# Kernel tuning notes

Hardware: AMD Instinct MI355X
Metric: run time of the kernel (lower is better)

Reference implementation:

```python
import jax, jax.numpy as jnp
import numpy as np

K = 16                      # instance ids 1..K (0 = background, ignored)
DELTA_V, DELTA_D, GAMMA = 0.5, 1.5, 0.001
W_CLUST, W_CENTER, W_BOUND, W_LOVASZ = 0.1, 0.1, 0.05, 0.01


def _pdist(x, y):
    # x: [..., n, d], y: [..., m, d] -> euclidean distances [..., n, m]
    x2 = (x * x).sum(-1)[..., :, None]
    y2 = (y * y).sum(-1)[..., None, :]
    d2 = x2 + y2 - 2.0 * jnp.einsum('...nd,...md->...nm', x, y)
    return jnp.sqrt(jnp.maximum(d2, 0.0))


def _losses(points, embeddings, labels):
    # F.normalize(embeddings, p=2, dim=2)
    emb = embeddings / jnp.maximum(
        jnp.linalg.norm(embeddings, axis=-1, keepdims=True), 1e-12)
    B, N, D = emb.shape
    ids = jnp.arange(1, K + 1)
    M = (labels[..., None] == ids).astype(emb.dtype)            # [B,N,K]
    cnt = M.sum(1)                                               # [B,K] (>=1 by construction)
    # raw per-instance feature centers (mean of normalized embeddings)
    fc = jnp.einsum('bnk,bnd->bkd', M, emb) / cnt[..., None]     # [B,K,D]
    cen = fc / jnp.maximum(jnp.linalg.norm(fc, axis=-1, keepdims=True), 1e-12)

    # ---- clustering: variance term ----
    d_nc = _pdist(emb, cen)                                      # [B,N,K]
    var_loss = ((jnp.maximum(d_nc - DELTA_V, 0.0) * M).sum(1) / cnt).sum() / (B + 1e-6)

    # ---- clustering: inter-center distance term ----
    cd = _pdist(cen, cen)                                        # [B,K,K]
    off = 1.0 - jnp.eye(K, dtype=emb.dtype)
    dist_loss = ((jnp.maximum(2.0 * DELTA_D - cd, 0.0) * off).sum((1, 2))
                 / (K * (K - 1))).sum() / (B + 1e-6)

    # ---- clustering: regularizer (Frobenius norm of centers) ----
    reg_loss = jnp.linalg.norm(cen.reshape(B, -1), axis=1).sum() * GAMMA / (B + 1e-6)

    # ---- center loss: spatial dist * feature dist to per-instance means ----
    gc = jnp.einsum('bnk,bnc->bkc', M, points) / cnt[..., None]  # geometric centers [B,K,3]
    sd = _pdist(points, gc)                                      # [B,N,K]
    fd = _pdist(emb, fc)                                         # [B,N,K] (fc NOT renormalized)
    center_loss = ((sd * fd * M).sum(1) / cnt).sum() / B

    # ---- boundary loss: full NxN cdist, zero same-instance entries ----
    dm = _pdist(emb, emb)                                        # [B,N,N]
    same = labels[:, :, None] == labels[:, None, :]
    bd = dm * (~same).astype(emb.dtype)
    boundary_loss = jnp.maximum(DELTA_D - bd, 0.0).mean(axis=(1, 2)).sum() / B

    enorm = jnp.maximum(jnp.linalg.norm(emb, axis=-1), 1e-8)     # [B,N]
    mnorm = jnp.maximum(jnp.linalg.norm(fc, axis=-1), 1e-8)      # [B,K]
    sim = jnp.einsum('bnd,bkd->bnk', emb, fc) / (enorm[..., None] * mnorm[:, None, :])
    order = jnp.argsort(-sim, axis=1)                            # descending sort per (b,k)
    ss = jnp.take_along_axis(sim, order, axis=1)                 # sorted similarities
    sm = jnp.take_along_axis(M, order, axis=1)                   # masks in sorted order
    inter = cnt[:, None, :] - jnp.cumsum(sm, axis=1)
    union = cnt[:, None, :] + jnp.cumsum(1.0 - sm, axis=1)
    jac = 1.0 - inter / union
    jd = jnp.concatenate([jac[:, :1], jac[:, 1:] - jac[:, :-1]], axis=1)
    lovasz_loss = (jnp.maximum(ss, 0.0) * jd).sum() / B

    total = (W_CLUST * (var_loss + dist_loss + reg_loss)
             + W_CENTER * center_loss + W_BOUND * boundary_loss
             + W_LOVASZ * lovasz_loss)
    return jnp.stack([total, var_loss, dist_loss, reg_loss,
                      center_loss, boundary_loss, lovasz_loss])


def setup_inputs() -> dict:
    key = jax.random.key(0)
    k1, k2, k3 = jax.random.split(key, 3)
    B, N, D = 4, 4096, 64
    points = jax.random.normal(k1, (B, N, 3), jnp.float32)
    embeddings = jax.random.normal(k2, (B, N, D), jnp.float32)
    labels = jax.random.randint(k3, (B, N), 0, K + 1)
    # guarantee every id 0..K appears in each cloud (matches torch unique() set)
    labels = labels.at[:, :K + 1].set(jnp.arange(K + 1))
    return {"points": points, "embeddings": embeddings, "instance_labels": labels}


def reference(points, embeddings, instance_labels):
    # returns stacked [total, var, dist, reg, center, boundary, lovasz]
    return _losses(points, embeddings, instance_labels)
```

## Files before the change

kernel.cpp:

```cpp
#include <hip/hip_runtime.h>

#define BB 4
#define NN 4096
#define DD 64
#define KK 16
#define NBUCK 2048
#define NCHB 144
#define NBND (NCHB * BB)
#define NLV1 256

#define OFF_EMB   0u
#define OFF_NRM2  1048576u
#define OFF_PFC   1064960u
#define OFF_PGC   1327104u
#define OFF_PCNT  1339392u
#define OFF_FC    1343488u
#define OFF_CEN   1347584u
#define OFF_GC    1351680u
#define OFF_FCN   1351872u
#define OFF_FCN2  1351936u
#define OFF_CEN2  1352000u
#define OFF_GC2   1352064u
#define OFF_CNTF  1352128u
#define OFF_BND   1352192u
#define OFF_VAR   1352768u
#define OFF_CENL  1353024u
#define OFF_LOV   1353280u
#define OFF_PH    OFF_PFC
#define OFF_EMBH  1354496u

typedef __attribute__((ext_vector_type(8))) short bf16x8;
typedef __attribute__((ext_vector_type(4))) float f32x4;

#define FSQRT(x) __builtin_amdgcn_sqrtf(x)
#define FRCP(x)  __builtin_amdgcn_rcpf(x)
#define FRSQ(x)  __builtin_amdgcn_rsqf(x)

__device__ __forceinline__ ushort f2bf(float x){
  unsigned u = __float_as_uint(x);
  return (ushort)((u + 0x7FFFu + ((u >> 16) & 1u)) >> 16);
}

__device__ __forceinline__ float blockReduceSum(float v, float* sbuf){
  int t = threadIdx.x;
  #pragma unroll
  for (int off = 32; off > 0; off >>= 1) v += __shfl_xor(v, off, 64);
  if ((t & 63) == 0) sbuf[t >> 6] = v;
  __syncthreads();
  float s = 0.f;
  if (t == 0){
    int nw = blockDim.x >> 6;
    for (int i = 0; i < nw; i++) s += sbuf[i];
  }
  __syncthreads();
  return s;
}

__device__ __forceinline__ double blockReduceD(double v, double* sbuf){
  int t = threadIdx.x;
  #pragma unroll
  for (int off = 32; off > 0; off >>= 1) v += __shfl_xor(v, off, 64);
  if ((t & 63) == 0) sbuf[t >> 6] = v;
  __syncthreads();
  double s = 0.0;
  if (t == 0){
    for (int i = 0; i < 4; i++) s += sbuf[i];
  }
  __syncthreads();
  return s;
}

__global__ void knormacc(const float* __restrict__ emb, const float* __restrict__ pts,
                         const int* __restrict__ lbl, float* __restrict__ ws){
  __shared__ float fcl[KK * DD];
  __shared__ float gcl[KK * 3];
  __shared__ float cntl[KK];
  int t = threadIdx.x;
  for (int i = t; i < KK * DD; i += 256) fcl[i] = 0.f;
  if (t < KK * 3) gcl[t] = 0.f;
  if (t < KK) cntl[t] = 0.f;
  __syncthreads();

  int lane = t & 63, w = t >> 6;
  int b = blockIdx.x >> 6;
  int local = blockIdx.x & 63;
  int base = local * 64 + w * 16;
  const float* E = emb + (size_t)b * NN * DD;
  float* EN = ws + OFF_EMB + (size_t)b * NN * DD;
  ushort* EH = (ushort*)(ws + OFF_EMBH) + (size_t)b * NN * DD;

  for (int i = 0; i < 16; i++){
    int n = base + i;
    float v = E[(size_t)n * DD + lane];
    float ss = v * v;
    #pragma unroll
    for (int off = 1; off < 64; off <<= 1) ss += __shfl_xor(ss, off, 64);
    float nrm = FSQRT(ss);
    float scale = FRCP(fmaxf(nrm, 1e-12f));
    float vn = v * scale;
    EN[(size_t)n * DD + lane] = vn;
    EH[(size_t)n * DD + lane] = f2bf(vn);
    if (lane == 0) ws[OFF_NRM2 + b * NN + n] = ss * scale * scale;
    int l = lbl[b * NN + n];
    if (l >= 1 && l <= KK){
      int k = l - 1;
      atomicAdd(&fcl[k * DD + lane], vn);
      if (lane < 3) atomicAdd(&gcl[k * 3 + lane], pts[((size_t)b * NN + n) * 3 + lane]);
      if (lane == 0) atomicAdd(&cntl[k], 1.0f);
    }
  }
  __syncthreads();
  for (int i = t; i < KK * DD; i += 256)
    ws[OFF_PFC + (size_t)blockIdx.x * KK * DD + i] = fcl[i];
  if (t < KK * 3) ws[OFF_PGC + blockIdx.x * KK * 3 + t] = gcl[t];
  if (t < KK)     ws[OFF_PCNT + blockIdx.x * KK + t] = cntl[t];
}

__global__ void kcenters(float* __restrict__ ws){
  __shared__ float accL[4][DD];
  int bk = blockIdx.x;
  int b = bk >> 4, k = bk & 15;
  int t = threadIdx.x;
  int lane = t & 63, w = t >> 6;
  float s = 0.f;
  #pragma unroll
  for (int j = 0; j < 16; j++)
    s += ws[OFF_PFC + (size_t)((b * 64 + w * 16 + j) * KK + k) * DD + lane];
  accL[w][lane] = s;
  __syncthreads();
  float fsum = 0.f, cp = 0.f, gp0 = 0.f, gp1 = 0.f, gp2 = 0.f;
  if (w == 0){
    fsum = accL[0][lane] + accL[1][lane] + accL[2][lane] + accL[3][lane];
    cp  = ws[OFF_PCNT + (b * 64 + lane) * KK + k];
    gp0 = ws[OFF_PGC + ((b * 64 + lane) * KK + k) * 3 + 0];
    gp1 = ws[OFF_PGC + ((b * 64 + lane) * KK + k) * 3 + 1];
    gp2 = ws[OFF_PGC + ((b * 64 + lane) * KK + k) * 3 + 2];
    #pragma unroll
    for (int off = 1; off < 64; off <<= 1){
      cp  += __shfl_xor(cp, off, 64);
      gp0 += __shfl_xor(gp0, off, 64);
      gp1 += __shfl_xor(gp1, off, 64);
      gp2 += __shfl_xor(gp2, off, 64);
    }
  }
  __syncthreads();
  for (int i = t; i < 4096; i += 256) ws[OFF_PH + bk * 4096 + i] = 0.f;
  if (w == 0){
    float inv_c = FRCP(cp);
    float f = fsum * inv_c;
    ws[OFF_FC + (size_t)(b * KK + k) * DD + lane] = f;
    float n2 = f * f;
    #pragma unroll
    for (int off = 1; off < 64; off <<= 1) n2 += __shfl_xor(n2, off, 64);
    float fn = FSQRT(n2);
    float inv = FRCP(fmaxf(fn, 1e-12f));
    float ce = f * inv;
    ws[OFF_CEN + (size_t)(b * KK + k) * DD + lane] = ce;
    float g0 = gp0 * inv_c, g1 = gp1 * inv_c, g2 = gp2 * inv_c;
    if (lane == 0){
      ws[OFF_GC + (b * KK + k) * 3 + 0] = g0;
      ws[OFF_GC + (b * KK + k) * 3 + 1] = g1;
      ws[OFF_GC + (b * KK + k) * 3 + 2] = g2;
      ws[OFF_FCN  + b * KK + k] = fn;
      ws[OFF_FCN2 + b * KK + k] = n2;
      ws[OFF_CEN2 + b * KK + k] = n2 * inv * inv;
      ws[OFF_GC2  + b * KK + k] = g0 * g0 + g1 * g1 + g2 * g2;
      ws[OFF_CNTF + b * KK + k] = cp;
    }
  }
}

__global__ __launch_bounds__(256, 4) void kfused(const int* __restrict__ lbl,
                                                 const ushort* __restrict__ EHg,
                                                 const float* __restrict__ pts,
                                                 float* __restrict__ ws){
  __shared__ float fcS[DD];
  __shared__ float red[16];
  int t = threadIdx.x;

  if (blockIdx.x < NLV1){
    int bk = blockIdx.x >> 2, part = blockIdx.x & 3;
    int b = bk >> 4, k = bk & 15;
    if (t < DD) fcS[t] = ws[OFF_FC + (size_t)(b * KK + k) * DD + t];
    float fcn   = ws[OFF_FCN  + b * KK + k];
    float fcn2  = ws[OFF_FCN2 + b * KK + k];
    float cen2  = ws[OFF_CEN2 + b * KK + k];
    float gc2   = ws[OFF_GC2  + b * KK + k];
    float g0    = ws[OFF_GC + (b * KK + k) * 3 + 0];
    float g1    = ws[OFF_GC + (b * KK + k) * 3 + 1];
    float g2v   = ws[OFF_GC + (b * KK + k) * 3 + 2];
    float invC  = FRCP(ws[OFF_CNTF + b * KK + k]);
    float invmfn = FRCP(fmaxf(fcn, 1e-8f));
    float invfc  = FRCP(fmaxf(fcn, 1e-12f));
    __syncthreads();

    unsigned* H = (unsigned*)(ws + OFF_PH) + bk * 4096;
    float* S = ws + OFF_PH + bk * 4096 + 2048;
    const float* EN = ws + OFF_EMB + (size_t)b * NN * DD;
    const float* NR = ws + OFF_NRM2 + b * NN;
    const int* LB = lbl + b * NN;
    float varA = 0.f, cenA = 0.f;

    for (int c = 0; c < 4; c++){
      int n = part * 1024 + c * 256 + t;
      const float4* e4 = (const float4*)&EN[(size_t)n * DD];
      float dx = 0.f, dy = 0.f, dz = 0.f, dw = 0.f;
      #pragma unroll
      for (int i = 0; i < 16; i++){
        float4 e = e4[i];
        float4 f = ((const float4*)fcS)[i];
        dx += e.x * f.x; dy += e.y * f.y; dz += e.z * f.z; dw += e.w * f.w;
      }
      float dot = (dx + dy) + (dz + dw);
      float nrm2 = NR[n];
      float sim = dot * FRSQ(nrm2) * invmfn;
      int m = (LB[n] == k + 1) ? 1 : 0;
      if (sim > 0.f){
        int q = (int)(sim * (float)NBUCK);
        q = q > NBUCK - 1 ? NBUCK - 1 : q;
        int qi = NBUCK - 1 - q;
        atomicAdd(&H[qi], 1u + ((unsigned)m << 16));
        atomicAdd(&S[qi], sim);
      }
      if (m){
        float dotc = dot * invfc;
        float dnc = FSQRT(fmaxf(nrm2 + cen2 - 2.f * dotc, 0.f));
        varA += fmaxf(dnc - 0.5f, 0.f);
        float fd = FSQRT(fmaxf(nrm2 + fcn2 - 2.f * dot, 0.f));
        float p0 = pts[((size_t)b * NN + n) * 3 + 0];
        float p1 = pts[((size_t)b * NN + n) * 3 + 1];
        float p2 = pts[((size_t)b * NN + n) * 3 + 2];
        float sd2 = p0 * p0 + p1 * p1 + p2 * p2 + gc2 - 2.f * (p0 * g0 + p1 * g1 + p2 * g2v);
        cenA += FSQRT(fmaxf(sd2, 0.f)) * fd;
      }
    }
    float vs = blockReduceSum(varA * invC, red);
    if (t == 0) ws[OFF_VAR + blockIdx.x] = vs;
    float cs = blockReduceSum(cenA * invC, red);
    if (t == 0) ws[OFF_CENL + blockIdx.x] = cs;
  } else {
    int q = blockIdx.x - NLV1;
    int b = q / NCHB;
    int cq = q - b * NCHB;
    int ti = 0, rem = cq;
    while (rem >= ((32 - ti + 3) >> 2)){ rem -= (32 - ti + 3) >> 2; ti++; }
    int tj0 = ti + rem * 4;
    int nt = 32 - tj0; if (nt > 4) nt = 4;

    int lane = t & 63, w = t >> 6;
    int lm = lane & 15;
    int rif = (lane >> 4) * 4;
    int lk = (lane >> 4) * 8;
    const ushort* E = EHg + (size_t)b * NN * DD;
    const float* NR = ws + OFF_NRM2 + b * NN;
    const int* LB = lbl + b * NN;

    bf16x8 a[2][2];
    #pragma unroll
    for (int rb = 0; rb < 2; rb++)
      #pragma unroll
      for (int kh = 0; kh < 2; kh++)
        a[rb][kh] = *(const bf16x8*)&E[(size_t)(ti * 128 + w * 32 + rb * 16 + lm) * DD + kh * 32 + lk];

    float nAr[8]; int lAr[8];
    #pragma unroll
    for (int rb = 0; rb < 2; rb++)
      #pragma unroll
      for (int r = 0; r < 4; r++){
        int gi = ti * 128 + w * 32 + rb * 16 + rif + r;
        nAr[rb * 4 + r] = NR[gi];
        lAr[rb * 4 + r] = LB[gi];
      }

    float sum = 0.f;
    for (int tt = 0; tt < nt; tt++){
      int tj = tj0 + tt;
      bool diag = (tj == ti);
      #pragma unroll
      for (int pass = 0; pass < 2; pass++){
        float nBr[4]; int lBr[4];
        #pragma unroll
        for (int cb = 0; cb < 4; cb++){
          int gj = tj * 128 + (pass * 4 + cb) * 16 + lm;
          nBr[cb] = NR[gj];
          lBr[cb] = LB[gj];
        }
        f32x4 ac[2][4];
        #pragma unroll
        for (int rb = 0; rb < 2; rb++)
          #pragma unroll
          for (int cb = 0; cb < 4; cb++) ac[rb][cb] = (f32x4){0.f, 0.f, 0.f, 0.f};
        #pragma unroll
        for (int cb = 0; cb < 4; cb++){
          #pragma unroll
          for (int kh = 0; kh < 2; kh++){
            bf16x8 bb = *(const bf16x8*)&E[(size_t)(tj * 128 + (pass * 4 + cb) * 16 + lm) * DD + kh * 32 + lk];
            ac[0][cb] = __builtin_amdgcn_mfma_f32_16x16x32_bf16(a[0][kh], bb, ac[0][cb], 0, 0, 0);
            ac[1][cb] = __builtin_amdgcn_mfma_f32_16x16x32_bf16(a[1][kh], bb, ac[1][cb], 0, 0, 0);
          }
        }
        if (diag){
          #pragma unroll
          for (int rb = 0; rb < 2; rb++)
            #pragma unroll
            for (int cb = 0; cb < 4; cb++)
              #pragma unroll
              for (int r = 0; r < 4; r++){
                float d2 = fmaxf(nAr[rb * 4 + r] + nBr[cb] - 2.f * ac[rb][cb][r], 0.f);
                if (lAr[rb * 4 + r] == lBr[cb]) d2 = 0.f;
                float f = fmaxf(1.5f - FSQRT(d2), 0.f);
                int gi = w * 32 + rb * 16 + rif + r;
                int gj = (pass * 4 + cb) * 16 + lm;
                sum += (gi < gj) ? f : 0.f;
              }
        } else {
          #pragma unroll
          for (int rb = 0; rb < 2; rb++)
            #pragma unroll
            for (int cb = 0; cb < 4; cb++)
              #pragma unroll
              for (int r = 0; r < 4; r++){
                float d2 = fmaxf(nAr[rb * 4 + r] + nBr[cb] - 2.f * ac[rb][cb][r], 0.f);
                if (lAr[rb * 4 + r] == lBr[cb]) d2 = 0.f;
                sum += fmaxf(1.5f - FSQRT(d2), 0.f);
              }
        }
      }
    }
    float s = blockReduceSum(sum, red);
    if (t == 0) ws[OFF_BND + q] = s;
  }
}

__global__ void klov2(float* __restrict__ ws){
  __shared__ unsigned wsum[4];
  __shared__ float red[16];
  int bk = blockIdx.x;
  int b = bk >> 4, k = bk & 15;
  int t = threadIdx.x;
  int lane = t & 63, w = t >> 6;
  const unsigned* H = (const unsigned*)(ws + OFF_PH) + bk * 4096;
  const float* S = ws + OFF_PH + bk * 4096 + 2048;
  float C = ws[OFF_CNTF + b * KK + k];

  int base = t * 8;
  unsigned hv[8]; float sv[8];
  #pragma unroll
  for (int i = 0; i < 8; i++){ hv[i] = H[base + i]; sv[i] = S[base + i]; }
  unsigned loc[8];
  unsigned run = 0;
  #pragma unroll
  for (int i = 0; i < 8; i++){ loc[i] = run; run += hv[i]; }
  unsigned tot = run, sc = tot;
  #pragma unroll
  for (int off = 1; off < 64; off <<= 1){
    unsigned v = __shfl_up(sc, off, 64);
    if (lane >= off) sc += v;
  }
  if (lane == 63) wsum[w] = sc;
  __syncthreads();
  unsigned wbase = 0;
  #pragma unroll
  for (int w2 = 0; w2 < 4; w2++) if (w2 < w) wbase += wsum[w2];
  unsigned ex = wbase + sc - tot;

  float contrib = 0.f;
  #pragma unroll
  for (int i = 0; i < 8; i++){
    unsigned h = hv[i];
    unsigned g = h & 0xFFFFu, mu = h >> 16;
    if (g){
      unsigned pre = ex + loc[i];
      float i0 = (float)(pre & 0xFFFFu), c0 = (float)(pre >> 16);
      float i1 = i0 + (float)g, c1 = c0 + (float)mu;
      float jac0 = 1.f - (C - c0) * FRCP(C + i0 - c0);
      float jac1 = 1.f - (C - c1) * FRCP(C + i1 - c1);
      contrib += sv[i] * (jac1 - jac0) * FRCP((float)g);
    }
  }
  float ls = blockReduceSum(contrib, red);
  if (t == 0) ws[OFF_LOV + bk] = ls;
}

__global__ void kfinal(const float* __restrict__ ws, float* __restrict__ out){
  __shared__ double dred[4];
  __shared__ float red[16];
  int t = threadIdx.x;
  double bs = 0.0;
  for (int i = t; i < NBND; i += 256) bs += (double)ws[OFF_BND + i];
  bs = blockReduceD(bs, dred);
  double lv = (t < 64) ? (double)ws[OFF_LOV + t] : 0.0;
  lv = blockReduceD(lv, dred);
  double va = (double)ws[OFF_VAR + t];
  va = blockReduceD(va, dred);
  double ce = (double)ws[OFF_CENL + t];
  ce = blockReduceD(ce, dred);

  double di = 0.0, rg = 0.0;
  int i = t >> 4, j = t & 15;
  for (int b = 0; b < BB; b++){
    float v = 0.f;
    if (i != j){
      float dot = 0.f;
      #pragma unroll
      for (int d = 0; d < DD; d++)
        dot += ws[OFF_CEN + (size_t)(b * KK + i) * DD + d] * ws[OFF_CEN + (size_t)(b * KK + j) * DD + d];
      float cd = FSQRT(fmaxf(ws[OFF_CEN2 + b * KK + i] + ws[OFF_CEN2 + b * KK + j] - 2.f * dot, 0.f));
      v = fmaxf(3.f - cd, 0.f);
    }
    float s = blockReduceSum(v, red);
    if (t == 0){
      di += (double)(s / 240.f);
      float s2 = 0.f;
      for (int k = 0; k < KK; k++) s2 += ws[OFF_CEN2 + b * KK + k];
      rg += (double)(FSQRT(s2) * 0.001f);
    }
  }
  if (t == 0){
    double var_l  = va / (4.0 + 1e-6);
    double dist_l = di / (4.0 + 1e-6);
    double reg_l  = rg / (4.0 + 1e-6);
    double cen_l  = ce / 4.0;
    double bnd_l  = (2.0 * bs + 1.5 * (double)NN * BB) / ((double)NN * NN * BB);
    double lov_l  = lv / 4.0;
    double total = 0.1 * (var_l + dist_l + reg_l) + 0.1 * cen_l + 0.05 * bnd_l + 0.01 * lov_l;
    out[0] = (float)total; out[1] = (float)var_l; out[2] = (float)dist_l;
    out[3] = (float)reg_l; out[4] = (float)cen_l; out[5] = (float)bnd_l;
    out[6] = (float)lov_l;
  }
}

extern "C" void kernel_launch(void* const* d_in, const int* in_sizes, int n_in,
                              void* d_out, int out_size, void* d_ws, size_t ws_size,
                              hipStream_t stream){
  const float* pts = (const float*)d_in[0];
  const float* emb = (const float*)d_in[1];
  const int* lbl   = (const int*)d_in[2];
  float* out = (float*)d_out;
  float* ws = (float*)d_ws;

  hipLaunchKernelGGL(knormacc, dim3(256), dim3(256), 0, stream, emb, pts, lbl, ws);
  hipLaunchKernelGGL(kcenters, dim3(64),  dim3(256), 0, stream, ws);
  hipLaunchKernelGGL(kfused,   dim3(NLV1 + NBND), dim3(256), 0, stream,
                     lbl, (const ushort*)(ws + OFF_EMBH), pts, ws);
  hipLaunchKernelGGL(klov2,    dim3(64),  dim3(256), 0, stream, ws);
  hipLaunchKernelGGL(kfinal,   dim3(1),   dim3(256), 0, stream, ws, out);
}
```

Before: 86.59 us.

## Restructure lovasz/variance pass to one thread per point looping over all instances

The per-instance pass no longer launches 256 blocks, each re-reading a quarter of one cloud's embeddings for a single instance. It now launches 64 blocks in which each thread loads its point's 64-float embedding into registers once and loops over all 16 instance centers. This cuts embedding traffic by a factor of 16. The costs are high register pressure from holding the embedding (which may lower occupancy under launch bounds), per-k center loads from global/L1, and scattered histogram atomics across all instances. The histogram buffer moves to its own workspace region so it no longer aliases the partial-center buffer, and kcenters drops one barrier.

```diff
diff --git a/kernel.cpp b/kernel.cpp
--- a/kernel.cpp
+++ b/kernel.cpp
@@ -7,7 +7,7 @@
 #define NBUCK 2048
 #define NCHB 144
 #define NBND (NCHB * BB)
-#define NLV1 256
+#define NLOV 64
 
 #define OFF_EMB   0u
 #define OFF_NRM2  1048576u
@@ -24,10 +24,10 @@
 #define OFF_CNTF  1352128u
 #define OFF_BND   1352192u
 #define OFF_VAR   1352768u
-#define OFF_CENL  1353024u
-#define OFF_LOV   1353280u
-#define OFF_PH    OFF_PFC
-#define OFF_EMBH  1354496u
+#define OFF_CENL  1352832u
+#define OFF_LOV   1352896u
+#define OFF_PH    1353216u
+#define OFF_EMBH  1615360u
 
 typedef __attribute__((ext_vector_type(8))) short bf16x8;
 typedef __attribute__((ext_vector_type(4))) float f32x4;
@@ -128,13 +128,13 @@
     s += ws[OFF_PFC + (size_t)((b * 64 + w * 16 + j) * KK + k) * DD + lane];
   accL[w][lane] = s;
   __syncthreads();
-  float fsum = 0.f, cp = 0.f, gp0 = 0.f, gp1 = 0.f, gp2 = 0.f;
+  for (int i = t; i < 4096; i += 256) ws[OFF_PH + bk * 4096 + i] = 0.f;
   if (w == 0){
-    fsum = accL[0][lane] + accL[1][lane] + accL[2][lane] + accL[3][lane];
-    cp  = ws[OFF_PCNT + (b * 64 + lane) * KK + k];
-    gp0 = ws[OFF_PGC + ((b * 64 + lane) * KK + k) * 3 + 0];
-    gp1 = ws[OFF_PGC + ((b * 64 + lane) * KK + k) * 3 + 1];
-    gp2 = ws[OFF_PGC + ((b * 64 + lane) * KK + k) * 3 + 2];
+    float fsum = accL[0][lane] + accL[1][lane] + accL[2][lane] + accL[3][lane];
+    float cp  = ws[OFF_PCNT + (b * 64 + lane) * KK + k];
+    float gp0 = ws[OFF_PGC + ((b * 64 + lane) * KK + k) * 3 + 0];
+    float gp1 = ws[OFF_PGC + ((b * 64 + lane) * KK + k) * 3 + 1];
+    float gp2 = ws[OFF_PGC + ((b * 64 + lane) * KK + k) * 3 + 2];
     #pragma unroll
     for (int off = 1; off < 64; off <<= 1){
       cp  += __shfl_xor(cp, off, 64);
@@ -142,10 +142,6 @@
       gp1 += __shfl_xor(gp1, off, 64);
       gp2 += __shfl_xor(gp2, off, 64);
     }
-  }
-  __syncthreads();
-  for (int i = t; i < 4096; i += 256) ws[OFF_PH + bk * 4096 + i] = 0.f;
-  if (w == 0){
     float inv_c = FRCP(cp);
     float f = fsum * inv_c;
     ws[OFF_FC + (size_t)(b * KK + k) * DD + lane] = f;
@@ -174,72 +170,78 @@
                                                  const ushort* __restrict__ EHg,
                                                  const float* __restrict__ pts,
                                                  float* __restrict__ ws){
-  __shared__ float fcS[DD];
   __shared__ float red[16];
   int t = threadIdx.x;
 
-  if (blockIdx.x < NLV1){
-    int bk = blockIdx.x >> 2, part = blockIdx.x & 3;
-    int b = bk >> 4, k = bk & 15;
-    if (t < DD) fcS[t] = ws[OFF_FC + (size_t)(b * KK + k) * DD + t];
-    float fcn   = ws[OFF_FCN  + b * KK + k];
-    float fcn2  = ws[OFF_FCN2 + b * KK + k];
-    float cen2  = ws[OFF_CEN2 + b * KK + k];
-    float gc2   = ws[OFF_GC2  + b * KK + k];
-    float g0    = ws[OFF_GC + (b * KK + k) * 3 + 0];
-    float g1    = ws[OFF_GC + (b * KK + k) * 3 + 1];
-    float g2v   = ws[OFF_GC + (b * KK + k) * 3 + 2];
-    float invC  = FRCP(ws[OFF_CNTF + b * KK + k]);
-    float invmfn = FRCP(fmaxf(fcn, 1e-8f));
-    float invfc  = FRCP(fmaxf(fcn, 1e-12f));
+  if (blockIdx.x < NLOV){
+    __shared__ float invmfnS[KK], invfcS[KK], invCS[KK], fcn2S[KK], cen2S[KK], gc2S[KK];
+    __shared__ float gcS[KK][3];
+    int g = blockIdx.x * 256 + t;
+    int b = g >> 12;
+    int n = g & (NN - 1);
+    if (t < KK){
+      float fcn = ws[OFF_FCN + b * KK + t];
+      invmfnS[t] = FRCP(fmaxf(fcn, 1e-8f));
+      invfcS[t]  = FRCP(fmaxf(fcn, 1e-12f));
+      invCS[t]   = FRCP(ws[OFF_CNTF + b * KK + t]);
+      fcn2S[t]   = ws[OFF_FCN2 + b * KK + t];
+      cen2S[t]   = ws[OFF_CEN2 + b * KK + t];
+      gc2S[t]    = ws[OFF_GC2  + b * KK + t];
+      gcS[t][0]  = ws[OFF_GC + (b * KK + t) * 3 + 0];
+      gcS[t][1]  = ws[OFF_GC + (b * KK + t) * 3 + 1];
+      gcS[t][2]  = ws[OFF_GC + (b * KK + t) * 3 + 2];
+    }
     __syncthreads();
 
-    unsigned* H = (unsigned*)(ws + OFF_PH) + bk * 4096;
-    float* S = ws + OFF_PH + bk * 4096 + 2048;
-    const float* EN = ws + OFF_EMB + (size_t)b * NN * DD;
-    const float* NR = ws + OFF_NRM2 + b * NN;
-    const int* LB = lbl + b * NN;
+    const float* EN = ws + OFF_EMB + (size_t)(b * NN + n) * DD;
+    float4 e4[16];
+    #pragma unroll
+    for (int i = 0; i < 16; i++) e4[i] = *(const float4*)&EN[i * 4];
+    float nrm2 = ws[OFF_NRM2 + b * NN + n];
+    float rs = FRSQ(nrm2);
+    int l = lbl[b * NN + n];
+    float p0 = pts[((size_t)b * NN + n) * 3 + 0];
+    float p1 = pts[((size_t)b * NN + n) * 3 + 1];
+    float p2 = pts[((size_t)b * NN + n) * 3 + 2];
+    float p2sum = p0 * p0 + p1 * p1 + p2 * p2;
     float varA = 0.f, cenA = 0.f;
 
-    for (int c = 0; c < 4; c++){
-      int n = part * 1024 + c * 256 + t;
-      const float4* e4 = (const float4*)&EN[(size_t)n * DD];
+    for (int k = 0; k < KK; k++){
+      const float* FCk = ws + OFF_FC + (size_t)(b * KK + k) * DD;
       float dx = 0.f, dy = 0.f, dz = 0.f, dw = 0.f;
       #pragma unroll
       for (int i = 0; i < 16; i++){
-        float4 e = e4[i];
-        float4 f = ((const float4*)fcS)[i];
-        dx += e.x * f.x; dy += e.y * f.y; dz += e.z * f.z; dw += e.w * f.w;
+        float4 f = *(const float4*)&FCk[i * 4];
+        dx += e4[i].x * f.x; dy += e4[i].y * f.y;
+        dz += e4[i].z * f.z; dw += e4[i].w * f.w;
       }
       float dot = (dx + dy) + (dz + dw);
-      float nrm2 = NR[n];
-      float sim = dot * FRSQ(nrm2) * invmfn;
-      int m = (LB[n] == k + 1) ? 1 : 0;
+      float sim = dot * rs * invmfnS[k];
+      int m = (l == k + 1) ? 1 : 0;
       if (sim > 0.f){
         int q = (int)(sim * (float)NBUCK);
         q = q > NBUCK - 1 ? NBUCK - 1 : q;
         int qi = NBUCK - 1 - q;
+        unsigned* H = (unsigned*)(ws + OFF_PH) + (size_t)(b * KK + k) * 4096;
+        float* S = ws + OFF_PH + (size_t)(b * KK + k) * 4096 + 2048;
         atomicAdd(&H[qi], 1u + ((unsigned)m << 16));
         atomicAdd(&S[qi], sim);
       }
       if (m){
-        float dotc = dot * invfc;
-        float dnc = FSQRT(fmaxf(nrm2 + cen2 - 2.f * dotc, 0.f));
-        varA += fmaxf(dnc - 0.5f, 0.f);
-        float fd = FSQRT(fmaxf(nrm2 + fcn2 - 2.f * dot, 0.f));
-        float p0 = pts[((size_t)b * NN + n) * 3 + 0];
-        float p1 = pts[((size_t)b * NN + n) * 3 + 1];
-        float p2 = pts[((size_t)b * NN + n) * 3 + 2];
-        float sd2 = p0 * p0 + p1 * p1 + p2 * p2 + gc2 - 2.f * (p0 * g0 + p1 * g1 + p2 * g2v);
-        cenA += FSQRT(fmaxf(sd2, 0.f)) * fd;
+        float dotc = dot * invfcS[k];
+        float dnc = FSQRT(fmaxf(nrm2 + cen2S[k] - 2.f * dotc, 0.f));
+        varA += fmaxf(dnc - 0.5f, 0.f) * invCS[k];
+        float fd = FSQRT(fmaxf(nrm2 + fcn2S[k] - 2.f * dot, 0.f));
+        float sd2 = p2sum + gc2S[k] - 2.f * (p0 * gcS[k][0] + p1 * gcS[k][1] + p2 * gcS[k][2]);
+        cenA += FSQRT(fmaxf(sd2, 0.f)) * fd * invCS[k];
       }
     }
-    float vs = blockReduceSum(varA * invC, red);
+    float vs = blockReduceSum(varA, red);
     if (t == 0) ws[OFF_VAR + blockIdx.x] = vs;
-    float cs = blockReduceSum(cenA * invC, red);
+    float cs = blockReduceSum(cenA, red);
     if (t == 0) ws[OFF_CENL + blockIdx.x] = cs;
   } else {
-    int q = blockIdx.x - NLV1;
+    int q = blockIdx.x - NLOV;
     int b = q / NCHB;
     int cq = q - b * NCHB;
     int ti = 0, rem = cq;
@@ -339,8 +341,8 @@
   int b = bk >> 4, k = bk & 15;
   int t = threadIdx.x;
   int lane = t & 63, w = t >> 6;
-  const unsigned* H = (const unsigned*)(ws + OFF_PH) + bk * 4096;
-  const float* S = ws + OFF_PH + bk * 4096 + 2048;
+  const unsigned* H = (const unsigned*)(ws + OFF_PH) + (size_t)bk * 4096;
+  const float* S = ws + OFF_PH + (size_t)bk * 4096 + 2048;
   float C = ws[OFF_CNTF + b * KK + k];
 
   int base = t * 8;
@@ -391,9 +393,9 @@
   bs = blockReduceD(bs, dred);
   double lv = (t < 64) ? (double)ws[OFF_LOV + t] : 0.0;
   lv = blockReduceD(lv, dred);
-  double va = (double)ws[OFF_VAR + t];
+  double va = (t < 64) ? (double)ws[OFF_VAR + t] : 0.0;
   va = blockReduceD(va, dred);
-  double ce = (double)ws[OFF_CENL + t];
+  double ce = (t < 64) ? (double)ws[OFF_CENL + t] : 0.0;
   ce = blockReduceD(ce, dred);
 
   double di = 0.0, rg = 0.0;
@@ -441,7 +443,7 @@
 
   hipLaunchKernelGGL(knormacc, dim3(256), dim3(256), 0, stream, emb, pts, lbl, ws);
   hipLaunchKernelGGL(kcenters, dim3(64),  dim3(256), 0, stream, ws);
-  hipLaunchKernelGGL(kfused,   dim3(NLV1 + NBND), dim3(256), 0, stream,
+  hipLaunchKernelGGL(kfused,   dim3(NLOV + NBND), dim3(256), 0, stream,
                      lbl, (const ushort*)(ws + OFF_EMBH), pts, ws);
   hipLaunchKernelGGL(klov2,    dim3(64),  dim3(256), 0, stream, ws);
   hipLaunchKernelGGL(kfinal,   dim3(1),   dim3(256), 0, stream, ws, out);
```

Result: faster. 77.77 us (median of 2 runs) (-10.2%).
